# Optimization experiments

Hardware: AMD Instinct MI355X
Metric: run time of the kernel (lower is better)

## Reference

```python
import jax, jax.numpy as jnp
import numpy as np

B, S, D, H = 4, 2048, 512, 8
E = D // H  # d_head = 64

def setup_inputs() -> dict:
    key = jax.random.key(0)
    ks = jax.random.split(key, 10)
    s_in = (1.0 / np.sqrt(D))
    x  = jax.random.normal(ks[0], (B, S, D), dtype=jnp.float32)
    Wq = jax.random.normal(ks[1], (H, D, E), dtype=jnp.float32) * s_in
    bq = jax.random.normal(ks[2], (H, E), dtype=jnp.float32) * 0.01
    Wk = jax.random.normal(ks[3], (H, D, E), dtype=jnp.float32) * s_in
    bk = jax.random.normal(ks[4], (H, E), dtype=jnp.float32) * 0.01
    Wv = jax.random.normal(ks[5], (H, D, E), dtype=jnp.float32) * s_in
    bv = jax.random.normal(ks[6], (H, E), dtype=jnp.float32) * 0.01
    Wo = jax.random.normal(ks[7], (D, D), dtype=jnp.float32) * s_in
    bo = jax.random.normal(ks[8], (D,), dtype=jnp.float32) * 0.01
    return {"x": x, "Wq": Wq, "bq": bq, "Wk": Wk, "bk": bk,
            "Wv": Wv, "bv": bv, "Wo": Wo, "bo": bo}

def reference(x, Wq, bq, Wk, bk, Wv, bv, Wo, bo):
    B_, S_, D_ = x.shape
    # per-head projections (batched over head axis h)
    q = jnp.einsum('bsd,hde->bhse', x, Wq) + bq[None, :, None, :]
    k = jnp.einsum('bsd,hde->bhse', x, Wk) + bk[None, :, None, :]
    v = jnp.einsum('bsd,hde->bhse', x, Wv) + bv[None, :, None, :]
    # NOTE: original scales by d_model**-0.5 (full D), not d_head**-0.5
    scale = jnp.asarray(D_, x.dtype) ** -0.5
    scores = jnp.einsum('bhse,bhte->bhst', q, k) * scale  # [B,H,S,S]
    causal = jnp.tril(jnp.ones((S_, S_), dtype=bool))
    scores = jnp.where(causal[None, None], scores, -jnp.inf)
    attn = jax.nn.softmax(scores, axis=-1)
    out = jnp.einsum('bhst,bhte->bhse', attn, v)  # [B,H,S,E]
    # concat heads along feature dim (head-major), matching torch.cat
    out = out.transpose(0, 2, 1, 3).reshape(B_, S_, D_)
    return out @ Wo + bo  # final projection; dropout never applied in source
```

## Files before the change

kernel.cpp:

```cpp
#include <hip/hip_runtime.h>

typedef unsigned short u16;
typedef __bf16 bf16x8 __attribute__((ext_vector_type(8)));
typedef short s16x4 __attribute__((ext_vector_type(4)));
typedef short s16x8 __attribute__((ext_vector_type(8)));
typedef float f32x4 __attribute__((ext_vector_type(4)));

#define BB 4
#define SS 2048
#define DD 512
#define HH 8
#define EE 64
#define MM 8192
#define BHSE (BB*HH*SS*EE)

#define GLOBAL_AS __attribute__((address_space(1)))
#define LDS_AS    __attribute__((address_space(3)))

__device__ __forceinline__ float b2f(u16 u) {
    return __uint_as_float(((unsigned int)u) << 16);
}
__device__ __forceinline__ u16 f2b(float f) {
    unsigned int v = __float_as_uint(f);
    v += 0x7fffu + ((v >> 16) & 1u);
    return (u16)(v >> 16);
}
__device__ __forceinline__ float loadE(const void* p, size_t idx, int isbf16) {
    return isbf16 ? b2f(((const u16*)p)[idx]) : ((const float*)p)[idx];
}
__device__ __forceinline__ f32x4 mfma16x16x16_bf16(s16x4 a, s16x4 b, f32x4 c) {
    return __builtin_amdgcn_mfma_f32_16x16x16bf16_1k(a, b, c, 0, 0, 0);
}
__device__ __forceinline__ void load_lds16(const u16* g, u16* l) {
    __builtin_amdgcn_global_load_lds((GLOBAL_AS void*)g, (LDS_AS void*)l, 16, 0, 0);
}

__device__ __forceinline__ int detect_bf16_wave(const u16* x) {
    const int lane = threadIdx.x & 63;
    float a0 = fabsf(b2f(x[2 * lane]));
    float a1 = fabsf(b2f(x[2 * (lane + 64)]));
    int c0 = (a0 == 0.f) || (a0 > 1e-4f && a0 < 100.f);
    int c1 = (a1 == 0.f) || (a1 > 1e-4f && a1 < 100.f);
    int cnt = __popcll(__ballot(c0)) + __popcll(__ballot(c1));
    return cnt >= 96;
}

__global__ __launch_bounds__(256) void prep(
    const void* __restrict__ X,
    const void* __restrict__ Wq, const void* __restrict__ Wk,
    const void* __restrict__ Wv, const void* __restrict__ Wo,
    u16* __restrict__ Xb, u16* __restrict__ WT, u16* __restrict__ WoT,
    int* __restrict__ flag)
{
    const int isbf16 = detect_bf16_wave((const u16*)X);
    const int bid = blockIdx.x;
    const int tid = threadIdx.x;
    if (bid < 1024) {
        if (bid == 0 && tid == 0) *flag = isbf16;
        const size_t i0 = ((size_t)bid * 256 + tid) * 16;
        if (isbf16) {
            const uint4* src = (const uint4*)(((const u16*)X) + i0);
            uint4* dst = (uint4*)(Xb + i0);
            dst[0] = src[0];
            dst[1] = src[1];
        } else {
            const float* xf = ((const float*)X) + i0;
            float4 f0 = *(const float4*)xf;
            float4 f1 = *(const float4*)(xf + 4);
            float4 f2 = *(const float4*)(xf + 8);
            float4 f3 = *(const float4*)(xf + 12);
            u16 tmp[16] = { f2b(f0.x), f2b(f0.y), f2b(f0.z), f2b(f0.w),
                            f2b(f1.x), f2b(f1.y), f2b(f1.z), f2b(f1.w),
                            f2b(f2.x), f2b(f2.y), f2b(f2.z), f2b(f2.w),
                            f2b(f3.x), f2b(f3.y), f2b(f3.z), f2b(f3.w) };
            *(uint4*)(Xb + i0) = *(const uint4*)tmp;
            *(uint4*)(Xb + i0 + 8) = *(const uint4*)(tmp + 8);
        }
        return;
    }
    const int j = bid - 1024;
    const int job = j >> 6;
    const int t = j & 63;
    const void* src; u16* dst; int src_ld;
    if (job < 3) {
        const void* W = (job == 0) ? Wq : ((job == 1) ? Wk : Wv);
        int h = t >> 3, kt = t & 7;
        size_t off = (size_t)h * DD * EE + (size_t)kt * 64 * EE;
        src = isbf16 ? (const void*)(((const u16*)W) + off)
                     : (const void*)(((const float*)W) + off);
        src_ld = EE;
        dst = WT + (size_t)job * 512 * 512 + (size_t)(h * 64) * 512 + kt * 64;
    } else {
        int a = t >> 3, b = t & 7;
        size_t off = (size_t)(a * 64) * 512 + b * 64;
        src = isbf16 ? (const void*)(((const u16*)Wo) + off)
                     : (const void*)(((const float*)Wo) + off);
        src_ld = 512;
        dst = WoT + (size_t)(b * 64) * 512 + a * 64;
    }
    __shared__ __align__(16) u16 Ts[64 * 72];
#pragma unroll
    for (int it = 0; it < 2; ++it) {
        int idx = it * 256 + tid;
        int r = idx >> 3, c = (idx & 7) << 3;
        u16 tmp[8];
        if (isbf16) {
            *(bf16x8*)tmp = *(const bf16x8*)(((const u16*)src) + (size_t)r * src_ld + c);
        } else {
            const float* sp = ((const float*)src) + (size_t)r * src_ld + c;
            float4 f0 = *(const float4*)sp;
            float4 f1 = *(const float4*)(sp + 4);
            tmp[0] = f2b(f0.x); tmp[1] = f2b(f0.y); tmp[2] = f2b(f0.z); tmp[3] = f2b(f0.w);
            tmp[4] = f2b(f1.x); tmp[5] = f2b(f1.y); tmp[6] = f2b(f1.z); tmp[7] = f2b(f1.w);
        }
#pragma unroll
        for (int k = 0; k < 8; ++k) Ts[(c + k) * 72 + r] = tmp[k];
    }
    __syncthreads();
#pragma unroll
    for (int it = 0; it < 2; ++it) {
        int idx = it * 256 + tid;
        int r = idx >> 3, c = (idx & 7) << 3;
        *(bf16x8*)(dst + (size_t)r * 512 + c) = *(const bf16x8*)&Ts[r * 72 + c];
    }
}

template<int MT, int NT>
__device__ __forceinline__ void mfma_step(const u16* As, const u16* Bs,
    int mh, int nh, int lq, int quad, f32x4 acc[MT][NT])
{
    const int sw = lq & 7;
#pragma unroll
    for (int kw = 0; kw < 2; ++kw) {
        const int G = kw * 4 + quad;
        const int col = ((G ^ sw) << 3);
        bf16x8 a[MT], b[NT];
#pragma unroll
        for (int mt = 0; mt < MT; ++mt)
            a[mt] = *(const bf16x8*)&As[(mh + mt * 16 + lq) * 64 + col];
#pragma unroll
        for (int nt = 0; nt < NT; ++nt)
            b[nt] = *(const bf16x8*)&Bs[(nh + nt * 16 + lq) * 64 + col];
#pragma unroll
        for (int mt = 0; mt < MT; ++mt)
#pragma unroll
            for (int nt = 0; nt < NT; ++nt)
                acc[mt][nt] = __builtin_amdgcn_mfma_f32_16x16x32_bf16(a[mt], b[nt], acc[mt][nt], 0, 0, 0);
    }
}

__global__ __launch_bounds__(256) void gemm_qkv(
    const u16* __restrict__ Xb, const u16* __restrict__ WT,
    const void* __restrict__ bq, const void* __restrict__ bk,
    const void* __restrict__ bv, u16* __restrict__ qkv,
    const int* __restrict__ flag)
{
    const float SCALE = 0.04419417382415922f;
    const int isbf16 = *flag;
    const int l = blockIdx.x;
    const int m0 = ((l & 7) * 8 + ((l >> 3) & 7)) * 128;
    const int n0 = (l >> 6) * 128;
    const int tid = threadIdx.x;
    const int wave = tid >> 6, lane = tid & 63;
    const int lq = lane & 15, quad = lane >> 4;
    const int mh = (wave & 1) * 64, nh = (wave >> 1) * 64;
    __shared__ __align__(16) u16 As[128 * 64];
    __shared__ __align__(16) u16 Bs[128 * 64];
    f32x4 acc[4][4] = {};

    const int swz = (lane & 7) ^ ((lane >> 3) & 7);
    const size_t lane_off = (size_t)(lane >> 3) * 512 + 8 * swz;

    for (int k0 = 0; k0 < 512; k0 += 64) {
        __syncthreads();
#pragma unroll
        for (int jj = 0; jj < 4; ++jj) {
            const int c = wave * 4 + jj;
            load_lds16(Xb + (size_t)(m0 + 8 * c) * 512 + k0 + lane_off, &As[c * 512]);
            load_lds16(WT + (size_t)(n0 + 8 * c) * 512 + k0 + lane_off, &Bs[c * 512]);
        }
        __syncthreads();
        mfma_step<4, 4>(As, Bs, mh, nh, lq, quad, acc);
    }

    const int proj = n0 >> 9;
    const void* bias = (proj == 0) ? bq : ((proj == 1) ? bk : bv);
#pragma unroll
    for (int mt = 0; mt < 4; ++mt) {
#pragma unroll
        for (int nt = 0; nt < 4; ++nt) {
#pragma unroll
            for (int r = 0; r < 4; ++r) {
                int m = m0 + mh + mt * 16 + quad * 4 + r;
                int n = n0 + nh + nt * 16 + lq;
                int nn = n & 511;
                float v = acc[mt][nt][r] + loadE(bias, nn, isbf16);
                if (proj == 0) v *= SCALE;
                int b_ = m >> 11, s = m & 2047, h = nn >> 6, e = nn & 63;
                qkv[(size_t)proj * BHSE + (((size_t)(b_ * HH + h) * SS + s) * EE + e)] = f2b(v);
            }
        }
    }
}

struct Stage { uint4 k0, k1, va, vb; };

__device__ __forceinline__ void stage_load(Stage& st, const u16* Kh, const u16* Vh,
                                           int t0, int tid) {
    int r = tid >> 3, c = (tid & 7) * 8;
    st.k0 = *(const uint4*)(Kh + (size_t)(t0 + r) * 64 + c);
    st.k1 = *(const uint4*)(Kh + (size_t)(t0 + r + 32) * 64 + c);
    int t2 = 2 * (tid & 31), e8 = (tid >> 5) * 8;
    st.va = *(const uint4*)(Vh + (size_t)(t0 + t2) * 64 + e8);
    st.vb = *(const uint4*)(Vh + (size_t)(t0 + t2 + 1) * 64 + e8);
}
__device__ __forceinline__ void stage_write(const Stage& st, u16* Ksb, u16* VTsb, int tid) {
    int r = tid >> 3, c = (tid & 7) * 8;
    *(uint4*)(Ksb + r * 72 + c) = st.k0;
    *(uint4*)(Ksb + (r + 32) * 72 + c) = st.k1;
    int t2 = 2 * (tid & 31), e8 = (tid >> 5) * 8;
    int g2 = ((t2 >> 2) & 3) * 16 + ((t2 >> 4) << 2) + (t2 & 3);
    const unsigned* pa = (const unsigned*)&st.va;
    const unsigned* pb = (const unsigned*)&st.vb;
#pragma unroll
    for (int k = 0; k < 4; ++k) {
        unsigned lo = __builtin_amdgcn_perm(pb[k], pa[k], 0x05040100u);
        unsigned hi = __builtin_amdgcn_perm(pb[k], pa[k], 0x07060302u);
        *(unsigned*)(VTsb + (e8 + 2 * k) * 72 + g2) = lo;
        *(unsigned*)(VTsb + (e8 + 2 * k + 1) * 72 + g2) = hi;
    }
}

__device__ __forceinline__ void attn_tile(const u16* Ksb, const u16* VTsb,
    bf16x8 qf0, bf16x8 qf1, int lq, int quad, int wave, bool diag,
    f32x4 Ot[4], f32x4& lfrag)
{
    const s16x4 ones = { (short)0x3F80, (short)0x3F80, (short)0x3F80, (short)0x3F80 };
#pragma unroll
    for (int half = 0; half < 2; ++half) {
        s16x4 vf[4][2];
#pragma unroll
        for (int et = 0; et < 4; ++et) {
            const u16* Vp = VTsb + (et * 16 + lq) * 72 + quad * 16 + half * 8;
            s16x8 v = *(const s16x8*)Vp;
            vf[et][0] = __builtin_shufflevector(v, v, 0, 1, 2, 3);
            vf[et][1] = __builtin_shufflevector(v, v, 4, 5, 6, 7);
        }
#pragma unroll
        for (int tj = 0; tj < 2; ++tj) {
            const int tt = half * 2 + tj;
            const u16* Krow = Ksb + (tt * 16 + lq) * 72;
            bf16x8 k0 = *(const bf16x8*)(Krow + quad * 8);
            bf16x8 k1 = *(const bf16x8*)(Krow + 32 + quad * 8);
            f32x4 sc = {};
            sc = __builtin_amdgcn_mfma_f32_16x16x32_bf16(k0, qf0, sc, 0, 0, 0);
            sc = __builtin_amdgcn_mfma_f32_16x16x32_bf16(k1, qf1, sc, 0, 0, 0);
            unsigned pu[4];
#pragma unroll
            for (int r = 0; r < 4; ++r) {
                float p = __expf(sc[r]);
                if (diag) {
                    int tl = tt * 16 + quad * 4 + r;
                    int ql = 16 * wave + lq;
                    p = (tl <= ql) ? p : 0.f;
                }
                pu[r] = __float_as_uint(p);
            }
            union { unsigned u[2]; s16x4 s; } pf;
            pf.u[0] = __builtin_amdgcn_perm(pu[1], pu[0], 0x07060302u);
            pf.u[1] = __builtin_amdgcn_perm(pu[3], pu[2], 0x07060302u);
            lfrag = mfma16x16x16_bf16(ones, pf.s, lfrag);
#pragma unroll
            for (int et = 0; et < 4; ++et)
                Ot[et] = mfma16x16x16_bf16(vf[et][tj], pf.s, Ot[et]);
        }
    }
}

__global__ __launch_bounds__(256) void attn_kernel(
    const u16* __restrict__ Qg, const u16* __restrict__ Kg,
    const u16* __restrict__ Vg, u16* __restrict__ Og,
    float* __restrict__ Opart, float* __restrict__ Lpart)
{
    const int bh = blockIdx.x;
    const int j  = (int)gridDim.y - 1 - (int)blockIdx.y;
    const int c  = blockIdx.z;
    if (c && j < 16) return;
    const int qb = j * 64;
    const int tFirst = c * 16;
    const int tLast  = (j < tFirst + 15) ? j : (tFirst + 15);
    const int nIt = tLast - tFirst;
    const bool diagHere = (tLast == j);
    const bool partial = (j >= 16);

    const int tid = threadIdx.x;
    const int wave = tid >> 6, lane = tid & 63;
    const int lq = lane & 15, quad = lane >> 4;
    const int b = bh >> 3, h = bh & 7;

    const size_t base = (size_t)bh * SS * EE;
    const u16* Kh = Kg + base;
    const u16* Vh = Vg + base;

    __shared__ __align__(16) u16 Ks[2][64 * 72];
    __shared__ __align__(16) u16 VTs[2][64 * 72];

    const int qrow = qb + 16 * wave + lq;
    const u16* Qp = Qg + base + (size_t)qrow * EE;
    bf16x8 qf0 = *(const bf16x8*)(Qp + quad * 8);
    bf16x8 qf1 = *(const bf16x8*)(Qp + 32 + quad * 8);

    f32x4 Ot[4] = {};
    f32x4 lfrag = {};

    Stage st;
    stage_load(st, Kh, Vh, tFirst * 64, tid);
    stage_write(st, Ks[0], VTs[0], tid);
    for (int i = 0; i <= nIt; ++i) {
        __syncthreads();
        const int cur = i & 1;
        const bool more = (i < nIt);
        if (more) stage_load(st, Kh, Vh, (tFirst + i + 1) * 64, tid);
        attn_tile(Ks[cur], VTs[cur], qf0, qf1, lq, quad, wave,
                  diagHere && (i == nIt), Ot, lfrag);
        if (more) stage_write(st, Ks[cur ^ 1], VTs[cur ^ 1], tid);
    }

    if (!partial) {
        const float inv = 1.f / lfrag[0];
        u16* Op = Og + (((size_t)(b * SS + qrow)) * HH + h) * EE;
#pragma unroll
        for (int et = 0; et < 4; ++et) {
            u16 tmp[4];
#pragma unroll
            for (int r = 0; r < 4; ++r) tmp[r] = f2b(Ot[et][r] * inv);
            *(uint2*)(Op + et * 16 + quad * 4) = *(const uint2*)tmp;
        }
    } else {
        const size_t slot = ((size_t)(bh * 16 + (j - 16)) * 2 + c);
        float* Os = Opart + slot * 4096;
        const int ql = 16 * wave + lq;
#pragma unroll
        for (int et = 0; et < 4; ++et)
            *(f32x4*)&Os[ql * 64 + et * 16 + quad * 4] = Ot[et];
        if (quad == 0) Lpart[slot * 64 + ql] = lfrag[0];
    }
}

__global__ __launch_bounds__(256) void attn_merge(
    const float* __restrict__ Opart, const float* __restrict__ Lpart,
    u16* __restrict__ Og)
{
    const int tg = blockIdx.x * 256 + threadIdx.x;
    const int e8 = (tg & 7) * 8;
    const int rest = tg >> 3;
    const int bh = rest >> 10;
    const int sp = rest & 1023;
    const int jj = sp >> 6;
    const int ql = sp & 63;
    const size_t slot = (size_t)(bh * 16 + jj) * 2;
    const size_t o0 = slot * 4096 + (size_t)ql * 64 + e8;
    float4 a0 = *(const float4*)&Opart[o0];
    float4 a1 = *(const float4*)&Opart[o0 + 4];
    float4 b0 = *(const float4*)&Opart[o0 + 4096];
    float4 b1 = *(const float4*)&Opart[o0 + 4096 + 4];
    const size_t ls = slot * 64 + ql;
    const float inv = 1.f / (Lpart[ls] + Lpart[ls + 64]);
    const int b = bh >> 3, h = bh & 7;
    const int s = 1024 + sp;
    u16 tmp[8];
    tmp[0] = f2b((a0.x + b0.x) * inv);
    tmp[1] = f2b((a0.y + b0.y) * inv);
    tmp[2] = f2b((a0.z + b0.z) * inv);
    tmp[3] = f2b((a0.w + b0.w) * inv);
    tmp[4] = f2b((a1.x + b1.x) * inv);
    tmp[5] = f2b((a1.y + b1.y) * inv);
    tmp[6] = f2b((a1.z + b1.z) * inv);
    tmp[7] = f2b((a1.w + b1.w) * inv);
    u16* Op = Og + (((size_t)(b * SS + s)) * HH + h) * EE + e8;
    *(uint4*)Op = *(const uint4*)tmp;
}

__global__ __launch_bounds__(256) void gemm_out(
    const u16* __restrict__ A, const u16* __restrict__ WoT,
    const void* __restrict__ bo, void* __restrict__ out,
    const int* __restrict__ flag)
{
    const int isbf16 = *flag;
    const int l = blockIdx.x;
    const int m0 = ((l & 7) * 8 + ((l >> 3) & 7)) * 128;
    const int n0 = (l >> 6) * 64;
    const int tid = threadIdx.x;
    const int wave = tid >> 6, lane = tid & 63;
    const int lq = lane & 15, quad = lane >> 4;
    const int mh = (wave & 1) * 64, nh = (wave >> 1) * 32;
    __shared__ __align__(16) u16 As[128 * 64];
    __shared__ __align__(16) u16 Bs[64 * 64];
    f32x4 acc[4][2] = {};

    const int swz = (lane & 7) ^ ((lane >> 3) & 7);
    const size_t lane_off = (size_t)(lane >> 3) * 512 + 8 * swz;

    for (int k0 = 0; k0 < 512; k0 += 64) {
        __syncthreads();
#pragma unroll
        for (int jj = 0; jj < 4; ++jj) {
            const int c = wave * 4 + jj;
            load_lds16(A + (size_t)(m0 + 8 * c) * 512 + k0 + lane_off, &As[c * 512]);
        }
#pragma unroll
        for (int jj = 0; jj < 2; ++jj) {
            const int c = wave * 2 + jj;
            load_lds16(WoT + (size_t)(n0 + 8 * c) * 512 + k0 + lane_off, &Bs[c * 512]);
        }
        __syncthreads();
        mfma_step<4, 2>(As, Bs, mh, nh, lq, quad, acc);
    }
#pragma unroll
    for (int mt = 0; mt < 4; ++mt) {
#pragma unroll
        for (int nt = 0; nt < 2; ++nt) {
#pragma unroll
            for (int r = 0; r < 4; ++r) {
                int m = m0 + mh + mt * 16 + quad * 4 + r;
                int n = n0 + nh + nt * 16 + lq;
                float v = acc[mt][nt][r] + loadE(bo, n, isbf16);
                if (isbf16) ((u16*)out)[(size_t)m * 512 + n] = f2b(v);
                else        ((float*)out)[(size_t)m * 512 + n] = v;
            }
        }
    }
}

extern "C" void kernel_launch(void* const* d_in, const int* in_sizes, int n_in,
                              void* d_out, int out_size, void* d_ws, size_t ws_size,
                              hipStream_t stream) {
    const void* x  = d_in[0];
    const void* Wq = d_in[1];
    const void* bq = d_in[2];
    const void* Wk = d_in[3];
    const void* bk = d_in[4];
    const void* Wv = d_in[5];
    const void* bv = d_in[6];
    const void* Wo = d_in[7];
    const void* bo = d_in[8];

    u16* WT   = (u16*)d_ws;
    u16* WoT  = WT + 3 * 512 * 512;
    u16* qkv  = WoT + 512 * 512;
    u16* attn = qkv + 3 * (size_t)BHSE;
    int* flag = (int*)(attn + (size_t)BHSE);
    u16* Xb   = (u16*)(flag + 8);
    float* Opart = (float*)(Xb + (size_t)MM * DD);
    float* Lpart = Opart + (size_t)1024 * 4096;

    prep<<<1024 + 256, 256, 0, stream>>>(x, Wq, Wk, Wv, Wo, Xb, WT, WoT, flag);
    gemm_qkv<<<(MM / 128) * (1536 / 128), 256, 0, stream>>>(Xb, WT, bq, bk, bv, qkv, flag);
    attn_kernel<<<dim3(BB * HH, SS / 64, 2), 256, 0, stream>>>(
        qkv, qkv + BHSE, qkv + 2 * (size_t)BHSE, attn, Opart, Lpart);
    attn_merge<<<1024, 256, 0, stream>>>(Opart, Lpart, attn);
    gemm_out<<<(MM / 128) * (512 / 64), 256, 0, stream>>>(attn, WoT, bo, d_out, flag);
}
```

Measured before the change: 184.3 us.

## Split attention tile across waves by query and key halves with LDS reduction

Each wave now handles 32 query rows against half of each 64-key tile, instead of 16 query rows against the full tile. K fragments are reused across two query fragments, and the PV and row-sum products move from 16x16x16 to 16x16x32 MFMAs. At the end the two key-half waves combine their partial O and l values through LDS before the write. This adds a reduction step with two extra barriers and raises register pressure, which the new launch bound of 4 is meant to contain.

```diff
diff --git a/kernel.cpp b/kernel.cpp
--- a/kernel.cpp
+++ b/kernel.cpp
@@ -27,9 +27,6 @@
 }
 __device__ __forceinline__ float loadE(const void* p, size_t idx, int isbf16) {
     return isbf16 ? b2f(((const u16*)p)[idx]) : ((const float*)p)[idx];
-}
-__device__ __forceinline__ f32x4 mfma16x16x16_bf16(s16x4 a, s16x4 b, f32x4 c) {
-    return __builtin_amdgcn_mfma_f32_16x16x16bf16_1k(a, b, c, 0, 0, 0);
 }
 __device__ __forceinline__ void load_lds16(const u16* g, u16* l) {
     __builtin_amdgcn_global_load_lds((GLOBAL_AS void*)g, (LDS_AS void*)l, 16, 0, 0);
@@ -231,53 +228,60 @@
     }
 }
 
-__device__ __forceinline__ void attn_tile(const u16* Ksb, const u16* VTsb,
-    bf16x8 qf0, bf16x8 qf1, int lq, int quad, int wave, bool diag,
-    f32x4 Ot[4], f32x4& lfrag)
-{
-    const s16x4 ones = { (short)0x3F80, (short)0x3F80, (short)0x3F80, (short)0x3F80 };
-#pragma unroll
-    for (int half = 0; half < 2; ++half) {
-        s16x4 vf[4][2];
-#pragma unroll
-        for (int et = 0; et < 4; ++et) {
-            const u16* Vp = VTsb + (et * 16 + lq) * 72 + quad * 16 + half * 8;
-            s16x8 v = *(const s16x8*)Vp;
-            vf[et][0] = __builtin_shufflevector(v, v, 0, 1, 2, 3);
-            vf[et][1] = __builtin_shufflevector(v, v, 4, 5, 6, 7);
-        }
-#pragma unroll
-        for (int tj = 0; tj < 2; ++tj) {
-            const int tt = half * 2 + tj;
-            const u16* Krow = Ksb + (tt * 16 + lq) * 72;
-            bf16x8 k0 = *(const bf16x8*)(Krow + quad * 8);
-            bf16x8 k1 = *(const bf16x8*)(Krow + 32 + quad * 8);
-            f32x4 sc = {};
-            sc = __builtin_amdgcn_mfma_f32_16x16x32_bf16(k0, qf0, sc, 0, 0, 0);
-            sc = __builtin_amdgcn_mfma_f32_16x16x32_bf16(k1, qf1, sc, 0, 0, 0);
-            unsigned pu[4];
+__device__ __forceinline__ void attn_tile2(const u16* Ksb, const u16* VTsb,
+    const bf16x8* qf0, const bf16x8* qf1, int lq, int quad, int qh, int th,
+    bool diag, f32x4 Ot[4][2], f32x4* lfrag)
+{
+    f32x4 sc[2][2];
+#pragma unroll
+    for (int tj = 0; tj < 2; ++tj) {
+        const u16* Krow = Ksb + ((th * 2 + tj) * 16 + lq) * 72;
+        bf16x8 k0 = *(const bf16x8*)(Krow + quad * 8);
+        bf16x8 k1 = *(const bf16x8*)(Krow + 32 + quad * 8);
+#pragma unroll
+        for (int f = 0; f < 2; ++f) {
+            f32x4 s = {};
+            s = __builtin_amdgcn_mfma_f32_16x16x32_bf16(k0, qf0[f], s, 0, 0, 0);
+            s = __builtin_amdgcn_mfma_f32_16x16x32_bf16(k1, qf1[f], s, 0, 0, 0);
+            sc[f][tj] = s;
+        }
+    }
+    union { unsigned u[4]; bf16x8 v; } ones;
+    ones.u[0] = ones.u[1] = ones.u[2] = ones.u[3] = 0x3F803F80u;
+    bf16x8 pf[2];
+#pragma unroll
+    for (int f = 0; f < 2; ++f) {
+        unsigned pu[8];
+#pragma unroll
+        for (int tj = 0; tj < 2; ++tj)
 #pragma unroll
             for (int r = 0; r < 4; ++r) {
-                float p = __expf(sc[r]);
+                float p = __expf(sc[f][tj][r]);
                 if (diag) {
-                    int tl = tt * 16 + quad * 4 + r;
-                    int ql = 16 * wave + lq;
+                    int tl = (th * 2 + tj) * 16 + quad * 4 + r;
+                    int ql = qh * 32 + f * 16 + lq;
                     p = (tl <= ql) ? p : 0.f;
                 }
-                pu[r] = __float_as_uint(p);
+                pu[tj * 4 + r] = __float_as_uint(p);
             }
-            union { unsigned u[2]; s16x4 s; } pf;
-            pf.u[0] = __builtin_amdgcn_perm(pu[1], pu[0], 0x07060302u);
-            pf.u[1] = __builtin_amdgcn_perm(pu[3], pu[2], 0x07060302u);
-            lfrag = mfma16x16x16_bf16(ones, pf.s, lfrag);
-#pragma unroll
-            for (int et = 0; et < 4; ++et)
-                Ot[et] = mfma16x16x16_bf16(vf[et][tj], pf.s, Ot[et]);
-        }
-    }
-}
-
-__global__ __launch_bounds__(256) void attn_kernel(
+        union { unsigned u[4]; bf16x8 v; } w;
+        w.u[0] = __builtin_amdgcn_perm(pu[1], pu[0], 0x07060302u);
+        w.u[1] = __builtin_amdgcn_perm(pu[3], pu[2], 0x07060302u);
+        w.u[2] = __builtin_amdgcn_perm(pu[5], pu[4], 0x07060302u);
+        w.u[3] = __builtin_amdgcn_perm(pu[7], pu[6], 0x07060302u);
+        pf[f] = w.v;
+        lfrag[f] = __builtin_amdgcn_mfma_f32_16x16x32_bf16(ones.v, w.v, lfrag[f], 0, 0, 0);
+    }
+#pragma unroll
+    for (int et = 0; et < 4; ++et) {
+        bf16x8 vf = *(const bf16x8*)(VTsb + (et * 16 + lq) * 72 + quad * 16 + th * 8);
+#pragma unroll
+        for (int f = 0; f < 2; ++f)
+            Ot[et][f] = __builtin_amdgcn_mfma_f32_16x16x32_bf16(vf, pf[f], Ot[et][f], 0, 0, 0);
+    }
+}
+
+__global__ __launch_bounds__(256, 4) void attn_kernel(
     const u16* __restrict__ Qg, const u16* __restrict__ Kg,
     const u16* __restrict__ Vg, u16* __restrict__ Og,
     float* __restrict__ Opart, float* __restrict__ Lpart)
@@ -296,6 +300,7 @@
     const int tid = threadIdx.x;
     const int wave = tid >> 6, lane = tid & 63;
     const int lq = lane & 15, quad = lane >> 4;
+    const int qh = wave & 1, th = wave >> 1;
     const int b = bh >> 3, h = bh & 7;
 
     const size_t base = (size_t)bh * SS * EE;
@@ -305,13 +310,17 @@
     __shared__ __align__(16) u16 Ks[2][64 * 72];
     __shared__ __align__(16) u16 VTs[2][64 * 72];
 
-    const int qrow = qb + 16 * wave + lq;
-    const u16* Qp = Qg + base + (size_t)qrow * EE;
-    bf16x8 qf0 = *(const bf16x8*)(Qp + quad * 8);
-    bf16x8 qf1 = *(const bf16x8*)(Qp + 32 + quad * 8);
-
-    f32x4 Ot[4] = {};
-    f32x4 lfrag = {};
+    bf16x8 qf0[2], qf1[2];
+#pragma unroll
+    for (int f = 0; f < 2; ++f) {
+        const int qrow_f = qb + qh * 32 + f * 16 + lq;
+        const u16* Qp = Qg + base + (size_t)qrow_f * EE;
+        qf0[f] = *(const bf16x8*)(Qp + quad * 8);
+        qf1[f] = *(const bf16x8*)(Qp + 32 + quad * 8);
+    }
+
+    f32x4 Ot[4][2] = {};
+    f32x4 lfrag[2] = {};
 
     Stage st;
     stage_load(st, Kh, Vh, tFirst * 64, tid);
@@ -321,29 +330,61 @@
         const int cur = i & 1;
         const bool more = (i < nIt);
         if (more) stage_load(st, Kh, Vh, (tFirst + i + 1) * 64, tid);
-        attn_tile(Ks[cur], VTs[cur], qf0, qf1, lq, quad, wave,
-                  diagHere && (i == nIt), Ot, lfrag);
+        attn_tile2(Ks[cur], VTs[cur], qf0, qf1, lq, quad, qh, th,
+                   diagHere && (i == nIt), Ot, lfrag);
         if (more) stage_write(st, Ks[cur ^ 1], VTs[cur ^ 1], tid);
     }
 
+    __syncthreads();
+    float* redO = (float*)&Ks[0][0];
+    float* redL = (float*)&VTs[0][0];
+    if (th == 1) {
+#pragma unroll
+        for (int et = 0; et < 4; ++et)
+#pragma unroll
+            for (int f = 0; f < 2; ++f)
+                *(f32x4*)&redO[(((qh * 4 + et) * 2 + f) * 64 + lane) * 4] = Ot[et][f];
+#pragma unroll
+        for (int f = 0; f < 2; ++f)
+            redL[(qh * 2 + f) * 64 + lane] = lfrag[f][0];
+    }
+    __syncthreads();
+    if (th == 1) return;
+    float lf[2];
+#pragma unroll
+    for (int f = 0; f < 2; ++f)
+        lf[f] = lfrag[f][0] + redL[(qh * 2 + f) * 64 + lane];
+#pragma unroll
+    for (int et = 0; et < 4; ++et)
+#pragma unroll
+        for (int f = 0; f < 2; ++f)
+            Ot[et][f] += *(const f32x4*)&redO[(((qh * 4 + et) * 2 + f) * 64 + lane) * 4];
+
     if (!partial) {
-        const float inv = 1.f / lfrag[0];
-        u16* Op = Og + (((size_t)(b * SS + qrow)) * HH + h) * EE;
-#pragma unroll
-        for (int et = 0; et < 4; ++et) {
-            u16 tmp[4];
-#pragma unroll
-            for (int r = 0; r < 4; ++r) tmp[r] = f2b(Ot[et][r] * inv);
-            *(uint2*)(Op + et * 16 + quad * 4) = *(const uint2*)tmp;
+#pragma unroll
+        for (int f = 0; f < 2; ++f) {
+            const float inv = 1.f / lf[f];
+            const int qrow_f = qb + qh * 32 + f * 16 + lq;
+            u16* Op = Og + (((size_t)(b * SS + qrow_f)) * HH + h) * EE;
+#pragma unroll
+            for (int et = 0; et < 4; ++et) {
+                u16 tmp[4];
+#pragma unroll
+                for (int r = 0; r < 4; ++r) tmp[r] = f2b(Ot[et][f][r] * inv);
+                *(uint2*)(Op + et * 16 + quad * 4) = *(const uint2*)tmp;
+            }
         }
     } else {
         const size_t slot = ((size_t)(bh * 16 + (j - 16)) * 2 + c);
         float* Os = Opart + slot * 4096;
-        const int ql = 16 * wave + lq;
-#pragma unroll
-        for (int et = 0; et < 4; ++et)
-            *(f32x4*)&Os[ql * 64 + et * 16 + quad * 4] = Ot[et];
-        if (quad == 0) Lpart[slot * 64 + ql] = lfrag[0];
+#pragma unroll
+        for (int f = 0; f < 2; ++f) {
+            const int ql = qh * 32 + f * 16 + lq;
+#pragma unroll
+            for (int et = 0; et < 4; ++et)
+                *(f32x4*)&Os[ql * 64 + et * 16 + quad * 4] = Ot[et][f];
+            if (quad == 0) Lpart[slot * 64 + ql] = lf[f];
+        }
     }
 }
 
```

Result: slower. 190.5 us (+3.4%).
